# Performance work log

Measured on AMD Instinct MI355X. Metric: run time of the kernel, lower is better.

Reference implementation:

```python
import jax, jax.numpy as jnp
import numpy as np

B = 131072
H_GAS = 8
H_EXT = 16
# gas order and net counts, total 99 tiny MLPs
GAS_SIZES = [23, 29, 13, 9, 3, 9, 13]  # h2o, h2o_sq, o3, co2, n2o, ch4, u
N_NETS = 29

# index maps taken verbatim from the 29 tau_gases assignment lines
H2O_ROWS = np.arange(23)
H2O_IDX = np.array([0,1,2,3,4,5,6,3,4,9,10,11,12,13,14,15,16,17,18,19,20,21,22])
O3_ROWS = np.array([0,1,2,17,18,19,20,21,22,25,26,27,28])
CO2_ROWS = np.array([0,1,2,5,6,9,10,13,14])
N2O_ROWS = np.array([0,1,2])
CH4_ROWS = np.array([0,1,2,3,4,7,8,11,12])
U_ROWS = np.array([0,1,2,15,16,17,18,19,20,21,22,27,28])


def setup_inputs() -> dict:
    key = jax.random.key(0)
    ks = jax.random.split(key, 23)
    f = jnp.float32
    inp = {
        'temp': jax.random.normal(ks[0], (B, 1), f),
        'pressure': jax.random.normal(ks[1], (B, 1), f),
        'comp_h2o': jax.random.uniform(ks[2], (B, 1), f),
        'comp_h2o_sq': jax.random.uniform(ks[3], (B, 1), f),
        'comp_o3': jax.random.uniform(ks[4], (B, 1), f),
        'comp_co2': jax.random.uniform(ks[5], (B, 1), f),
        'comp_n2o': jax.random.uniform(ks[6], (B, 1), f),
        'comp_ch4': jax.random.uniform(ks[7], (B, 1), f),
        'comp_u': jax.random.uniform(ks[8], (B, 1), f),
        'lwp': jax.random.uniform(ks[9], (B, 1), f, minval=0.05, maxval=1.0),
        'iwp': jax.random.uniform(ks[10], (B, 1), f, minval=0.05, maxval=1.0),
        'mu': jax.random.uniform(ks[11], (B, 1), f, minval=0.1, maxval=1.0),
        'mu_bar': jax.random.uniform(ks[12], (B, 1), f, minval=0.1, maxval=1.0),
        'gas_W1': jax.random.normal(ks[13], (99, 2, H_GAS), f) * 0.5,
        'gas_b1': jax.random.normal(ks[14], (99, H_GAS), f) * 0.1,
        'gas_W2': jax.random.normal(ks[15], (99, H_GAS, 1), f) * 0.5,
        'gas_b2': jax.random.uniform(ks[16], (99, 1), f, minval=0.05, maxval=0.5),
        'lw_w': jax.random.uniform(ks[17], (N_NETS, 1), f, minval=0.05, maxval=1.0),
        'iw_w': jax.random.uniform(ks[18], (N_NETS, 1), f, minval=0.05, maxval=1.0),
        'ext_W1': jax.random.normal(ks[19], (N_NETS, 4, H_EXT), f) * 0.5,
        'ext_b1': jax.random.normal(ks[20], (N_NETS, H_EXT), f) * 0.1,
        'ext_W2': jax.random.normal(ks[21], (N_NETS, H_EXT, 3), f) * 0.5,
        'ext_b2': jax.random.normal(ks[22], (N_NETS, 3), f) * 0.1,
    }
    return inp


def reference(temp, pressure, comp_h2o, comp_h2o_sq, comp_o3, comp_co2, comp_n2o,
              comp_ch4, comp_u, lwp, iwp, mu, mu_bar,
              gas_W1, gas_b1, gas_W2, gas_b2, lw_w, iw_w,
              ext_W1, ext_b1, ext_W2, ext_b2):
    b = temp.shape[0]
    X = jnp.concatenate([temp, pressure], axis=-1)              # [B,2]
    # all 99 per-gas tiny MLPs in one batched pass
    h = jax.nn.elu(jnp.einsum('bi,nih->nbh', X, gas_W1) + gas_b1[:, None, :])
    ke = jax.nn.relu(jnp.einsum('nbh,nho->nbo', h, gas_W2) + gas_b2[:, None, :])[..., 0]  # [99,B]
    comps = [comp_h2o, comp_h2o_sq, comp_o3, comp_co2, comp_n2o, comp_ch4, comp_u]
    comp_all = jnp.concatenate(
        [jnp.broadcast_to(c[:, 0][None, :], (n, b)) for c, n in zip(comps, GAS_SIZES)], axis=0)
    tau_all = ke * comp_all                                      # [99,B]
    h2o    = tau_all[0:23]
    h2o_sq = tau_all[23:52]
    o3     = tau_all[52:65]
    co2    = tau_all[65:74]
    n2o    = tau_all[74:77]
    ch4    = tau_all[77:86]
    u      = tau_all[86:99]
    # scatter-combine into the 29 spectral channels
    tau_g = h2o_sq                                               # every row has h2o_sq[k]
    tau_g = tau_g.at[H2O_ROWS].add(h2o[H2O_IDX])
    tau_g = tau_g.at[O3_ROWS].add(o3)
    tau_g = tau_g.at[CO2_ROWS].add(co2)
    tau_g = tau_g.at[N2O_ROWS].add(n2o)
    tau_g = tau_g.at[CH4_ROWS].add(ch4)
    tau_g = tau_g.at[U_ROWS].add(u)
    tau_lw = lw_w * lwp[:, 0][None, :]                           # [29,B]
    tau_iw = iw_w * iwp[:, 0][None, :]
    tau_total = tau_g + tau_lw + tau_iw
    in1 = tau_lw / tau_total
    in2 = tau_iw / tau_total
    mu_v, mub_v = mu[:, 0], mu_bar[:, 0]
    in3_dir = tau_total / mu_v[None, :]
    in3_dif = tau_total / mub_v[None, :]

    def ext(i1, i2, i3, m):
        Xe = jnp.stack([i1, i2, i3, jnp.broadcast_to(m[None, :], i1.shape)], axis=-1)  # [29,B,4]
        he = jax.nn.elu(jnp.einsum('nbi,nih->nbh', Xe, ext_W1) + ext_b1[:, None, :])
        return jax.nn.relu(jnp.einsum('nbh,nho->nbo', he, ext_W2) + ext_b2[:, None, :])

    e_direct = jax.nn.softmax(ext(in1, in2, in3_dir, mu_v), axis=-1)   # [29,B,3]
    e_diffuse = jax.nn.softmax(ext(in1, in2, in3_dif, mub_v), axis=-1)
    t_direct = jnp.exp(-in3_dir)
    t_diffuse = jnp.exp(-in3_dif)
    return (t_direct, t_diffuse, e_direct, e_diffuse)
```

## Files before the change

kernel.cpp:

```cpp
#include <hip/hip_runtime.h>
#include <math.h>

#define TPB 256
#define EPT 2

typedef float v2f __attribute__((ext_vector_type(2)));

#define VFMA(a, b, c) __builtin_elementwise_fma((a), (b), (c))
#define VMAX(a, b) __builtin_elementwise_max((a), (b))
#define VMIN(a, b) __builtin_elementwise_min((a), (b))
#define LOG2E 1.4426950408889634f

struct f3 { float a, b, c; };

struct Ptrs {
    const float *temp, *pressure;
    const float *c0, *c1, *c2, *c3, *c4, *c5, *c6;
    const float *lwp, *iwp, *mu, *mub;
    const float *gW1, *gb1, *gW2, *gb2;
    const float *lww, *iww;
    const float *eW1, *eb1, *eW2, *eb2;
    float* out;
    int Bn;
};

static __device__ __forceinline__ v2f sp(float s) { return (v2f){s, s}; }

static __device__ __forceinline__ float fexp2(float x) {
#if __has_builtin(__builtin_amdgcn_exp2f)
    return __builtin_amdgcn_exp2f(x);
#else
    return __expf(x * 0.6931471805599453f);
#endif
}

static __device__ __forceinline__ float fast_rcp(float x) {
    return __builtin_amdgcn_rcpf(x);
}

static __device__ __forceinline__ v2f elu2(v2f h) {
    v2f t = VMIN(h, sp(0.f)) * LOG2E;
    v2f e = {fexp2(t.x), fexp2(t.y)};
    return VMAX(h, sp(0.f)) + e - 1.0f;
}

static __device__ const unsigned char NETS[29][8] = {
    {  0, 23,  52,  65,  74,  77,  86, 255},
    {  1, 24,  53,  66,  75,  78,  87, 255},
    {  2, 25,  54,  67,  76,  79,  88, 255},
    {  3, 26, 255, 255, 255,  80, 255, 255},
    {  4, 27, 255, 255, 255,  81, 255, 255},
    {  5, 28, 255,  68, 255, 255, 255, 255},
    {  6, 29, 255,  69, 255, 255, 255, 255},
    {  3, 30, 255, 255, 255,  82, 255, 255},
    {  4, 31, 255, 255, 255,  83, 255, 255},
    {  9, 32, 255,  70, 255, 255, 255, 255},
    { 10, 33, 255,  71, 255, 255, 255, 255},
    { 11, 34, 255, 255, 255,  84, 255, 255},
    { 12, 35, 255, 255, 255,  85, 255, 255},
    { 13, 36, 255,  72, 255, 255, 255, 255},
    { 14, 37, 255,  73, 255, 255, 255, 255},
    { 15, 38, 255, 255, 255, 255,  89, 255},
    { 16, 39, 255, 255, 255, 255,  90, 255},
    { 17, 40,  55, 255, 255, 255,  91, 255},
    { 18, 41,  56, 255, 255, 255,  92, 255},
    { 19, 42,  57, 255, 255, 255,  93, 255},
    { 20, 43,  58, 255, 255, 255,  94, 255},
    { 21, 44,  59, 255, 255, 255,  95, 255},
    { 22, 45,  60, 255, 255, 255,  96, 255},
    {255, 46, 255, 255, 255, 255, 255, 255},
    {255, 47, 255, 255, 255, 255, 255, 255},
    {255, 48,  61, 255, 255, 255, 255, 255},
    {255, 49,  62, 255, 255, 255, 255, 255},
    {255, 50,  63, 255, 255, 255,  97, 255},
    {255, 51,  64, 255, 255, 255,  98, 255}};

static __device__ __forceinline__ void softmax3_v2(v2f o0, v2f o1, v2f o2,
                                                   v2f& r0, v2f& r1, v2f& r2) {
    o0 = VMAX(o0, sp(0.f));
    o1 = VMAX(o1, sp(0.f));
    o2 = VMAX(o2, sp(0.f));
    v2f mx = VMAX(o0, VMAX(o1, o2));
    v2f nm = mx * (-LOG2E);
    v2f a0 = VFMA(o0, sp(LOG2E), nm);
    v2f a1 = VFMA(o1, sp(LOG2E), nm);
    v2f a2 = VFMA(o2, sp(LOG2E), nm);
    v2f e0 = {fexp2(a0.x), fexp2(a0.y)};
    v2f e1 = {fexp2(a1.x), fexp2(a1.y)};
    v2f e2 = {fexp2(a2.x), fexp2(a2.y)};
    v2f ssum = e0 + e1 + e2;
    v2f rs = {fast_rcp(ssum.x), fast_rcp(ssum.y)};
    r0 = e0 * rs; r1 = e1 * rs; r2 = e2 * rs;
}

template <bool GUARD>
static __device__ __forceinline__ void item_body(const Ptrs& P, int r, int bA,
                                                 bool vB, int bBl) {
    const int Bn = P.Bn;

    const v2f t2  = {P.temp[bA],     P.temp[bBl]};
    const v2f p2  = {P.pressure[bA], P.pressure[bBl]};
    const v2f lwp2 = {P.lwp[bA], P.lwp[bBl]};
    const v2f iwp2 = {P.iwp[bA], P.iwp[bBl]};
    const v2f mu2  = {P.mu[bA],  P.mu[bBl]};
    const v2f mb2  = {P.mub[bA], P.mub[bBl]};

    v2f tg = sp(0.f);
    #pragma unroll
    for (int s = 0; s < 7; ++s) {
        const int n = NETS[r][s];
        if (n != 255) {
            const float* cp =
                (s == 0) ? P.c0 : (s == 1) ? P.c1 :
                (s == 2) ? P.c2 : (s == 3) ? P.c3 :
                (s == 4) ? P.c4 : (s == 5) ? P.c5 : P.c6;
            const v2f cs = {cp[bA], cp[bBl]};
            const float4* W1 = (const float4*)(P.gW1 + (n << 4));
            const float4 wt0 = W1[0], wt1 = W1[1];
            const float4 wp0 = W1[2], wp1 = W1[3];
            const float4* B1 = (const float4*)(P.gb1 + (n << 3));
            const float4 bb0 = B1[0], bb1 = B1[1];
            const float4* W2 = (const float4*)(P.gW2 + (n << 3));
            const float4 wo0 = W2[0], wo1 = W2[1];
            v2f acc = sp(P.gb2[n]);
#define GAS_H(WT, WP, BB, WO, K)                                            \
            { v2f h = VFMA(t2, sp((WT).K), VFMA(p2, sp((WP).K), sp((BB).K))); \
              h = elu2(h);                                                   \
              acc = VFMA(h, sp((WO).K), acc); }
            GAS_H(wt0, wp0, bb0, wo0, x)
            GAS_H(wt0, wp0, bb0, wo0, y)
            GAS_H(wt0, wp0, bb0, wo0, z)
            GAS_H(wt0, wp0, bb0, wo0, w)
            GAS_H(wt1, wp1, bb1, wo1, x)
            GAS_H(wt1, wp1, bb1, wo1, y)
            GAS_H(wt1, wp1, bb1, wo1, z)
            GAS_H(wt1, wp1, bb1, wo1, w)
#undef GAS_H
            acc = VMAX(acc, sp(0.f));
            tg = VFMA(acc, cs, tg);
        }
    }

    const float lwr = P.lww[r], iwr = P.iww[r];
    v2f tlw = lwp2 * lwr;
    v2f tiw = iwp2 * iwr;
    v2f tt = tg + tlw + tiw;
    v2f rtt = {fast_rcp(tt.x), fast_rcp(tt.y)};
    v2f in1 = tlw * rtt;
    v2f in2 = tiw * rtt;
    v2f rmu = {fast_rcp(mu2.x), fast_rcp(mu2.y)};
    v2f rmb = {fast_rcp(mb2.x), fast_rcp(mb2.y)};
    v2f i3d = tt * rmu;
    v2f i3f = tt * rmb;

    float* out = P.out;
    const int idxA = r * Bn + bA;
    {
        v2f ad = i3d * (-LOG2E);
        v2f af = i3f * (-LOG2E);
        out[idxA] = fexp2(ad.x);
        out[29 * Bn + idxA] = fexp2(af.x);
        if (!GUARD || vB) {
            out[idxA + TPB] = fexp2(ad.y);
            out[29 * Bn + idxA + TPB] = fexp2(af.y);
        }
    }

    const float* w1  = P.eW1 + (r << 6);
    const float* ebv = P.eb1 + (r << 4);
    const float* w2  = P.eW2 + r * 48;
    const float bo0 = P.eb2[r * 3 + 0];
    const float bo1 = P.eb2[r * 3 + 1];
    const float bo2 = P.eb2[r * 3 + 2];

    v2f d0 = sp(bo0), d1 = sp(bo1), d2 = sp(bo2);
    v2f f0 = sp(bo0), f1 = sp(bo1), f2 = sp(bo2);

    #pragma unroll
    for (int q = 0; q < 4; ++q) {
        const float4 wA4 = *(const float4*)(w1 + 4 * q);
        const float4 wB4 = *(const float4*)(w1 + 16 + 4 * q);
        const float4 wC4 = *(const float4*)(w1 + 32 + 4 * q);
        const float4 wD4 = *(const float4*)(w1 + 48 + 4 * q);
        const float4 bj4 = *(const float4*)(ebv + 4 * q);
        const float4 u0  = *(const float4*)(w2 + 12 * q);
        const float4 u1  = *(const float4*)(w2 + 12 * q + 4);
        const float4 u2  = *(const float4*)(w2 + 12 * q + 8);
#define EXT_H(K, W20, W21, W22)                                               \
        { v2f bs = VFMA(in1, sp((wA4).K), VFMA(in2, sp((wB4).K), sp((bj4).K))); \
          v2f hd = elu2(VFMA(i3d, sp((wC4).K), VFMA(mu2, sp((wD4).K), bs)));   \
          v2f hf = elu2(VFMA(i3f, sp((wC4).K), VFMA(mb2, sp((wD4).K), bs)));   \
          d0 = VFMA(hd, sp(W20), d0); d1 = VFMA(hd, sp(W21), d1);              \
          d2 = VFMA(hd, sp(W22), d2);                                          \
          f0 = VFMA(hf, sp(W20), f0); f1 = VFMA(hf, sp(W21), f1);              \
          f2 = VFMA(hf, sp(W22), f2); }
        EXT_H(x, u0.x, u0.y, u0.z)
        EXT_H(y, u0.w, u1.x, u1.y)
        EXT_H(z, u1.z, u1.w, u2.x)
        EXT_H(w, u2.y, u2.z, u2.w)
#undef EXT_H
    }

    v2f r0, r1, r2;
    softmax3_v2(d0, d1, d2, r0, r1, r2);
    f3* pdA = (f3*)(out + 58 * Bn) + idxA;
    pdA[0] = (f3){r0.x, r1.x, r2.x};
    if (!GUARD || vB) pdA[TPB] = (f3){r0.y, r1.y, r2.y};
    softmax3_v2(f0, f1, f2, r0, r1, r2);
    f3* pfA = (f3*)(out + 145 * Bn) + idxA;
    pfA[0] = (f3){r0.x, r1.x, r2.x};
    if (!GUARD || vB) pfA[TPB] = (f3){r0.y, r1.y, r2.y};
}

__global__ __launch_bounds__(TPB) void atm_persist(Ptrs P, int yshift,
                                                   int items, int stride) {
    const int ymask = (1 << yshift) - 1;
    for (int it = blockIdx.x; it < items; it += stride) {
        const int r = it >> yshift;
        const int bA = ((it & ymask) * (TPB * EPT)) + threadIdx.x;
        item_body<false>(P, r, bA, true, bA + TPB);
    }
}

template <bool GUARD>
__global__ __launch_bounds__(TPB) void atm_legacy(Ptrs P) {
    const int r = blockIdx.x;
    const int bA = blockIdx.y * (TPB * EPT) + threadIdx.x;
    if (GUARD && bA >= P.Bn) return;
    const int bB = bA + TPB;
    bool vB = true;
    int bBl = bB;
    if (GUARD) { vB = (bB < P.Bn); bBl = vB ? bB : bA; }
    item_body<GUARD>(P, r, bA, vB, bBl);
}

extern "C" void kernel_launch(void* const* d_in, const int* in_sizes, int n_in,
                              void* d_out, int out_size, void* d_ws, size_t ws_size,
                              hipStream_t stream) {
    const int Bn = in_sizes[0];
    Ptrs P;
    P.temp = (const float*)d_in[0];  P.pressure = (const float*)d_in[1];
    P.c0 = (const float*)d_in[2];    P.c1 = (const float*)d_in[3];
    P.c2 = (const float*)d_in[4];    P.c3 = (const float*)d_in[5];
    P.c4 = (const float*)d_in[6];    P.c5 = (const float*)d_in[7];
    P.c6 = (const float*)d_in[8];
    P.lwp = (const float*)d_in[9];   P.iwp = (const float*)d_in[10];
    P.mu = (const float*)d_in[11];   P.mub = (const float*)d_in[12];
    P.gW1 = (const float*)d_in[13];  P.gb1 = (const float*)d_in[14];
    P.gW2 = (const float*)d_in[15];  P.gb2 = (const float*)d_in[16];
    P.lww = (const float*)d_in[17];  P.iww = (const float*)d_in[18];
    P.eW1 = (const float*)d_in[19];  P.eb1 = (const float*)d_in[20];
    P.eW2 = (const float*)d_in[21];  P.eb2 = (const float*)d_in[22];
    P.out = (float*)d_out;
    P.Bn = Bn;

    const int span = TPB * EPT;
    if (Bn % span == 0) {
        const int yc = Bn / span;
        if ((yc & (yc - 1)) == 0) {
            int yshift = 0;
            while ((1 << yshift) != yc) ++yshift;
            const int items = 29 * yc;
            const int iters = (items + 2047) / 2048;
            const int grid  = (items + iters - 1) / iters;
            atm_persist<<<grid, TPB, 0, stream>>>(P, yshift, items, grid);
            return;
        }
        dim3 g(29, yc);
        atm_legacy<false><<<g, TPB, 0, stream>>>(P);
        return;
    }
    dim3 g(29, (Bn + span - 1) / span);
    atm_legacy<true><<<g, TPB, 0, stream>>>(P);
}
```

Baseline: 222.7 us.

## Use adjacent element pairs per thread with vectorized loads and stores

Each thread now handles two adjacent batch elements instead of two elements a block apart, so inputs load as float2 and the transmittance outputs store as float2. The seven composition inputs are loaded up front rather than inside the net loop. The persistent grid-stride kernel is dropped in favour of a plain 2D grid over (net, batch chunk). The adjacent f3 softmax stores become 24-byte contiguous per thread. The cost is more launched blocks and larger per-thread strides in the store pattern.

After: 215.0 us. 3.5% less time.

```diff
diff --git a/kernel.cpp b/kernel.cpp
--- a/kernel.cpp
+++ b/kernel.cpp
@@ -2,7 +2,6 @@
 #include <math.h>
 
 #define TPB 256
-#define EPT 2
 
 typedef float v2f __attribute__((ext_vector_type(2)));
 
@@ -82,39 +81,46 @@
     o2 = VMAX(o2, sp(0.f));
     v2f mx = VMAX(o0, VMAX(o1, o2));
     v2f nm = mx * (-LOG2E);
-    v2f a0 = VFMA(o0, sp(LOG2E), nm);
-    v2f a1 = VFMA(o1, sp(LOG2E), nm);
-    v2f a2 = VFMA(o2, sp(LOG2E), nm);
-    v2f e0 = {fexp2(a0.x), fexp2(a0.y)};
-    v2f e1 = {fexp2(a1.x), fexp2(a1.y)};
-    v2f e2 = {fexp2(a2.x), fexp2(a2.y)};
+    v2f x0 = VFMA(o0, sp(LOG2E), nm);
+    v2f x1 = VFMA(o1, sp(LOG2E), nm);
+    v2f x2 = VFMA(o2, sp(LOG2E), nm);
+    v2f e0 = {fexp2(x0.x), fexp2(x0.y)};
+    v2f e1 = {fexp2(x1.x), fexp2(x1.y)};
+    v2f e2 = {fexp2(x2.x), fexp2(x2.y)};
     v2f ssum = e0 + e1 + e2;
     v2f rs = {fast_rcp(ssum.x), fast_rcp(ssum.y)};
     r0 = e0 * rs; r1 = e1 * rs; r2 = e2 * rs;
 }
 
 template <bool GUARD>
-static __device__ __forceinline__ void item_body(const Ptrs& P, int r, int bA,
-                                                 bool vB, int bBl) {
+__global__ __launch_bounds__(TPB) void atm2(Ptrs P) {
+    const int r = blockIdx.x;
     const int Bn = P.Bn;
-
-    const v2f t2  = {P.temp[bA],     P.temp[bBl]};
-    const v2f p2  = {P.pressure[bA], P.pressure[bBl]};
-    const v2f lwp2 = {P.lwp[bA], P.lwp[bBl]};
-    const v2f iwp2 = {P.iwp[bA], P.iwp[bBl]};
-    const v2f mu2  = {P.mu[bA],  P.mu[bBl]};
-    const v2f mb2  = {P.mub[bA], P.mub[bBl]};
+    const int e0 = blockIdx.y * (2 * TPB) + 2 * threadIdx.x;
+    if (GUARD && e0 >= Bn) return;
+    const bool v1 = !GUARD || (e0 + 1 < Bn);
+    const int e1 = v1 ? e0 + 1 : e0;
+    const int gid = e0 >> 1;
+
+#define LD2(p) (GUARD ? (v2f){(p)[e0], (p)[e1]} \
+                      : *(const v2f*)((const float2*)(p) + gid))
+    const v2f t2  = LD2(P.temp);
+    const v2f p2  = LD2(P.pressure);
+    v2f comp2[7];
+    comp2[0] = LD2(P.c0); comp2[1] = LD2(P.c1); comp2[2] = LD2(P.c2);
+    comp2[3] = LD2(P.c3); comp2[4] = LD2(P.c4); comp2[5] = LD2(P.c5);
+    comp2[6] = LD2(P.c6);
+    const v2f lwp2 = LD2(P.lwp);
+    const v2f iwp2 = LD2(P.iwp);
+    const v2f mu2  = LD2(P.mu);
+    const v2f mb2  = LD2(P.mub);
+#undef LD2
 
     v2f tg = sp(0.f);
     #pragma unroll
     for (int s = 0; s < 7; ++s) {
         const int n = NETS[r][s];
         if (n != 255) {
-            const float* cp =
-                (s == 0) ? P.c0 : (s == 1) ? P.c1 :
-                (s == 2) ? P.c2 : (s == 3) ? P.c3 :
-                (s == 4) ? P.c4 : (s == 5) ? P.c5 : P.c6;
-            const v2f cs = {cp[bA], cp[bBl]};
             const float4* W1 = (const float4*)(P.gW1 + (n << 4));
             const float4 wt0 = W1[0], wt1 = W1[1];
             const float4 wp0 = W1[2], wp1 = W1[3];
@@ -137,7 +143,7 @@
             GAS_H(wt1, wp1, bb1, wo1, w)
 #undef GAS_H
             acc = VMAX(acc, sp(0.f));
-            tg = VFMA(acc, cs, tg);
+            tg = VFMA(acc, comp2[s], tg);
         }
     }
 
@@ -154,15 +160,22 @@
     v2f i3f = tt * rmb;
 
     float* out = P.out;
-    const int idxA = r * Bn + bA;
+    const int idx0 = r * Bn + e0;
     {
         v2f ad = i3d * (-LOG2E);
         v2f af = i3f * (-LOG2E);
-        out[idxA] = fexp2(ad.x);
-        out[29 * Bn + idxA] = fexp2(af.x);
-        if (!GUARD || vB) {
-            out[idxA + TPB] = fexp2(ad.y);
-            out[29 * Bn + idxA + TPB] = fexp2(af.y);
+        v2f td = {fexp2(ad.x), fexp2(ad.y)};
+        v2f tf = {fexp2(af.x), fexp2(af.y)};
+        if (!GUARD) {
+            *(v2f*)(out + idx0) = td;
+            *(v2f*)(out + 29 * Bn + idx0) = tf;
+        } else {
+            out[idx0] = td.x;
+            out[29 * Bn + idx0] = tf.x;
+            if (v1) {
+                out[idx0 + 1] = td.y;
+                out[29 * Bn + idx0 + 1] = tf.y;
+            }
         }
     }
 
@@ -203,35 +216,13 @@
 
     v2f r0, r1, r2;
     softmax3_v2(d0, d1, d2, r0, r1, r2);
-    f3* pdA = (f3*)(out + 58 * Bn) + idxA;
-    pdA[0] = (f3){r0.x, r1.x, r2.x};
-    if (!GUARD || vB) pdA[TPB] = (f3){r0.y, r1.y, r2.y};
+    f3* pd = (f3*)(out + 58 * Bn) + idx0;
+    pd[0] = (f3){r0.x, r1.x, r2.x};
+    if (v1) pd[1] = (f3){r0.y, r1.y, r2.y};
     softmax3_v2(f0, f1, f2, r0, r1, r2);
-    f3* pfA = (f3*)(out + 145 * Bn) + idxA;
-    pfA[0] = (f3){r0.x, r1.x, r2.x};
-    if (!GUARD || vB) pfA[TPB] = (f3){r0.y, r1.y, r2.y};
-}
-
-__global__ __launch_bounds__(TPB) void atm_persist(Ptrs P, int yshift,
-                                                   int items, int stride) {
-    const int ymask = (1 << yshift) - 1;
-    for (int it = blockIdx.x; it < items; it += stride) {
-        const int r = it >> yshift;
-        const int bA = ((it & ymask) * (TPB * EPT)) + threadIdx.x;
-        item_body<false>(P, r, bA, true, bA + TPB);
-    }
-}
-
-template <bool GUARD>
-__global__ __launch_bounds__(TPB) void atm_legacy(Ptrs P) {
-    const int r = blockIdx.x;
-    const int bA = blockIdx.y * (TPB * EPT) + threadIdx.x;
-    if (GUARD && bA >= P.Bn) return;
-    const int bB = bA + TPB;
-    bool vB = true;
-    int bBl = bB;
-    if (GUARD) { vB = (bB < P.Bn); bBl = vB ? bB : bA; }
-    item_body<GUARD>(P, r, bA, vB, bBl);
+    f3* pf = (f3*)(out + 145 * Bn) + idx0;
+    pf[0] = (f3){r0.x, r1.x, r2.x};
+    if (v1) pf[1] = (f3){r0.y, r1.y, r2.y};
 }
 
 extern "C" void kernel_launch(void* const* d_in, const int* in_sizes, int n_in,
@@ -254,22 +245,11 @@
     P.out = (float*)d_out;
     P.Bn = Bn;
 
-    const int span = TPB * EPT;
+    const int span = 2 * TPB;
+    dim3 g(29, (Bn + span - 1) / span);
     if (Bn % span == 0) {
-        const int yc = Bn / span;
-        if ((yc & (yc - 1)) == 0) {
-            int yshift = 0;
-            while ((1 << yshift) != yc) ++yshift;
-            const int items = 29 * yc;
-            const int iters = (items + 2047) / 2048;
-            const int grid  = (items + iters - 1) / iters;
-            atm_persist<<<grid, TPB, 0, stream>>>(P, yshift, items, grid);
-            return;
-        }
-        dim3 g(29, yc);
-        atm_legacy<false><<<g, TPB, 0, stream>>>(P);
-        return;
-    }
-    dim3 g(29, (Bn + span - 1) / span);
-    atm_legacy<true><<<g, TPB, 0, stream>>>(P);
-}
+        atm2<false><<<g, TPB, 0, stream>>>(P);
+    } else {
+        atm2<true><<<g, TPB, 0, stream>>>(P);
+    }
+}
```
